# Performance work log

Hardware: AMD Instinct MI355X
Metric: run time of the kernel (lower is better)

Reference implementation:

```python
import jax, jax.numpy as jnp
import numpy as np


def setup_inputs() -> dict:
    key = jax.random.key(0)
    k1, _ = jax.random.split(key)
    N = 4096
    states = jax.random.normal(k1, (N, 8), dtype=jnp.float32)
    log_tau = jnp.log(jnp.asarray(0.05, dtype=jnp.float32))
    return {"states": states, "log_tau": log_tau}


def reference(states, log_tau):
    N = states.shape[0]
    tau = jnp.exp(log_tau)
    pos = (states[:, :2] + states[:, 2:4]) / 2.0   # [N, 2]
    vel = (states[:, 4:6] + states[:, 6:8]) / 2.0  # [N, 2]
    dpos = pos[:, None, :] - pos[None, :, :]       # [N, N, 2]
    dvel = vel[:, None, :] - vel[None, :, :]       # [N, N, 2]
    f_ij = jnp.concatenate([dpos, dvel], axis=-1)  # [N, N, 4]
    dist = jnp.sqrt(jnp.sum(dpos ** 2, axis=-1) + 1e-08)  # [N, N]
    eye = jnp.eye(N, dtype=bool)
    logits = jnp.where(eye, -1e9, -dist / tau)
    alpha = jax.nn.softmax(logits, axis=-1)        # [N, N]
    mu = jnp.einsum('ij,ijd->id', alpha, f_ij)     # [N, 4]
    diff2 = (f_ij - mu[:, None, :]) ** 2           # [N, N, 4]
    sigma = jnp.sqrt(jnp.einsum('ij,ijd->id', alpha, diff2) + 1e-06)  # [N, 4]
    group_vel = jnp.broadcast_to(jnp.mean(vel, axis=0, keepdims=True), (N, 2))
    vel_dev = vel - group_vel
    return jnp.concatenate([mu, sigma, group_vel, vel_dev], axis=-1)  # [N, 12]
```

## Files before the change

kernel.cpp:

```cpp
#include <hip/hip_runtime.h>
#include <math.h>

typedef float v2f __attribute__((ext_vector_type(2)));

#define N_PTS 4096
#define BLOCK 512
#define RPB 4
#define CHUNK 2048
#define SLICES (BLOCK / RPB)
#define JPS (CHUNK / SLICES)
#define PPT (CHUNK / BLOCK)

__global__ __launch_bounds__(BLOCK, 6) void fused_kernel(
        const float* __restrict__ states,
        const float* __restrict__ log_tau_p,
        float* __restrict__ out) {
    __shared__ float4 pvs[CHUNK];
    __shared__ float wsum[8][2];
    __shared__ float red[8][RPB][10];

    const int tid  = threadIdx.x;
    const int lane = tid & 63;
    const int wave = tid >> 6;

    const float s    = __expf(-log_tau_p[0]) * 1.4426950408889634f;
    const float eps2 = 1e-8f * s * s;

    const int rowg = blockIdx.x * RPB + (lane & 3);
    const float4 r0 = *reinterpret_cast<const float4*>(states + rowg * 8);
    const float4 r1 = *reinterpret_cast<const float4*>(states + rowg * 8 + 4);
    const v2f pis = { (r0.x + r0.z) * 0.5f * s, (r0.y + r0.w) * 0.5f * s };
    const v2f piv = { (r1.x + r1.z) * 0.5f,     (r1.y + r1.w) * 0.5f };

    const int slice = wave * (SLICES / 8) + (lane >> 2);

    float l = 0.f, svx = 0.f, svy = 0.f;
    v2f S1p = {0.f, 0.f}, S1v = {0.f, 0.f}, S2p = {0.f, 0.f}, S2v = {0.f, 0.f};

    #pragma unroll
    for (int pass = 0; pass < N_PTS / CHUNK; ++pass) {
        const int J0 = pass * CHUNK;
        #pragma unroll
        for (int k = 0; k < PPT; ++k) {
            const int p = tid + k * BLOCK;
            const float4 s0 = *reinterpret_cast<const float4*>(states + (J0 + p) * 8);
            const float4 s1 = *reinterpret_cast<const float4*>(states + (J0 + p) * 8 + 4);
            float4 e;
            e.x = (s0.x + s0.z) * 0.5f * s;
            e.y = (s0.y + s0.w) * 0.5f * s;
            e.z = (s1.x + s1.z) * 0.5f;
            e.w = (s1.y + s1.w) * 0.5f;
            pvs[p] = e;
            svx += e.z; svy += e.w;
        }
        __syncthreads();

        #pragma unroll 8
        for (int tt = 0; tt < JPS; ++tt) {
            const float4 q = pvs[slice + tt * SLICES];
            v2f dp = { pis.x - q.x, pis.y - q.y };
            v2f dv = { piv.x - q.z, piv.y - q.w };
            float d2 = fmaf(dp.x, dp.x, fmaf(dp.y, dp.y, eps2));
            float w  = __builtin_amdgcn_exp2f(-__builtin_amdgcn_sqrtf(d2));
            l += w;
            v2f wv = { w, w };
            v2f t0 = dp * wv;
            v2f t1 = dv * wv;
            S1p += t0;
            S1v += t1;
            S2p += t0 * dp;
            S2v += t1 * dv;
        }
        __syncthreads();
    }

    float tx = svx, ty = svy;
    #pragma unroll
    for (int off = 32; off; off >>= 1) {
        tx += __shfl_down(tx, off);
        ty += __shfl_down(ty, off);
    }
    if (lane == 0) { wsum[wave][0] = tx; wsum[wave][1] = ty; }

    #pragma unroll
    for (int off = 4; off < 64; off <<= 1) {
        l     += __shfl_xor(l, off);
        S1p.x += __shfl_xor(S1p.x, off);
        S1p.y += __shfl_xor(S1p.y, off);
        S1v.x += __shfl_xor(S1v.x, off);
        S1v.y += __shfl_xor(S1v.y, off);
        S2p.x += __shfl_xor(S2p.x, off);
        S2p.y += __shfl_xor(S2p.y, off);
        S2v.x += __shfl_xor(S2v.x, off);
        S2v.y += __shfl_xor(S2v.y, off);
    }
    if (lane < RPB) {
        float* rr = red[wave][lane];
        rr[0] = l;
        rr[1] = S1p.x; rr[2] = S1p.y; rr[3] = S1v.x; rr[4] = S1v.y;
        rr[5] = S2p.x; rr[6] = S2p.y; rr[7] = S2v.x; rr[8] = S2v.y;
    }
    __syncthreads();

    if (tid < RPB) {
        float acc[9];
        #pragma unroll
        for (int cc = 0; cc < 9; ++cc) acc[cc] = red[0][tid][cc];
        #pragma unroll
        for (int wv = 1; wv < 8; ++wv)
            #pragma unroll
            for (int cc = 0; cc < 9; ++cc) acc[cc] += red[wv][tid][cc];

        const float w_diag = __builtin_amdgcn_exp2f(-__builtin_amdgcn_sqrtf(eps2));
        const float inv_l = 1.0f / (acc[0] - w_diag);
        const float inv_s = 1.0f / s;

        float gvx = 0.f, gvy = 0.f;
        #pragma unroll
        for (int wv = 0; wv < 8; ++wv) { gvx += wsum[wv][0]; gvy += wsum[wv][1]; }
        gvx *= (1.0f / N_PTS);
        gvy *= (1.0f / N_PTS);

        const int row = blockIdx.x * RPB + tid;
        const float4 q1 = *reinterpret_cast<const float4*>(states + row * 8 + 4);
        const float rvx = (q1.x + q1.z) * 0.5f;
        const float rvy = (q1.y + q1.w) * 0.5f;

        float mu[4], sg[4];
        mu[0] = acc[1] * inv_l * inv_s;
        mu[1] = acc[2] * inv_l * inv_s;
        mu[2] = acc[3] * inv_l;
        mu[3] = acc[4] * inv_l;
        const float inv_s2 = inv_s * inv_s;
        float e2[4];
        e2[0] = acc[5] * inv_l * inv_s2;
        e2[1] = acc[6] * inv_l * inv_s2;
        e2[2] = acc[7] * inv_l;
        e2[3] = acc[8] * inv_l;
        #pragma unroll
        for (int d = 0; d < 4; ++d)
            sg[d] = __builtin_amdgcn_sqrtf(fmaf(-mu[d], mu[d], e2[d]) + 1e-6f);

        float4* o = reinterpret_cast<float4*>(out + row * 12);
        o[0] = make_float4(mu[0], mu[1], mu[2], mu[3]);
        o[1] = make_float4(sg[0], sg[1], sg[2], sg[3]);
        o[2] = make_float4(gvx, gvy, rvx - gvx, rvy - gvy);
    }
}

extern "C" void kernel_launch(void* const* d_in, const int* in_sizes, int n_in,
                              void* d_out, int out_size, void* d_ws, size_t ws_size,
                              hipStream_t stream) {
    const float* states  = (const float*)d_in[0];
    const float* log_tau = (const float*)d_in[1];
    float* out = (float*)d_out;
    fused_kernel<<<N_PTS / RPB, BLOCK, 0, stream>>>(states, log_tau, out);
}
```

Before: 70.32 us.

## Register-block all four rows per thread to reuse each shared-memory load

Each thread now holds all four query rows in registers and loops over its own j points, so every float4 read from LDS is reused across four rows instead of one. This cuts LDS traffic by about four times relative to the math. The cost is much more register pressure (36 accumulators plus row data) under the launch bound of 6, and a longer end-of-kernel reduction, since every row now needs a full 64-lane shuffle reduction instead of a partial one.

```diff
diff --git a/kernel.cpp b/kernel.cpp
--- a/kernel.cpp
+++ b/kernel.cpp
@@ -7,9 +7,8 @@
 #define BLOCK 512
 #define RPB 4
 #define CHUNK 2048
-#define SLICES (BLOCK / RPB)
-#define JPS (CHUNK / SLICES)
 #define PPT (CHUNK / BLOCK)
+#define NPASS (N_PTS / CHUNK)
 
 __global__ __launch_bounds__(BLOCK, 6) void fused_kernel(
         const float* __restrict__ states,
@@ -17,7 +16,7 @@
         float* __restrict__ out) {
     __shared__ float4 pvs[CHUNK];
     __shared__ float wsum[8][2];
-    __shared__ float red[8][RPB][10];
+    __shared__ float red[8][RPB][9];
 
     const int tid  = threadIdx.x;
     const int lane = tid & 63;
@@ -26,19 +25,29 @@
     const float s    = __expf(-log_tau_p[0]) * 1.4426950408889634f;
     const float eps2 = 1e-8f * s * s;
 
-    const int rowg = blockIdx.x * RPB + (lane & 3);
-    const float4 r0 = *reinterpret_cast<const float4*>(states + rowg * 8);
-    const float4 r1 = *reinterpret_cast<const float4*>(states + rowg * 8 + 4);
-    const v2f pis = { (r0.x + r0.z) * 0.5f * s, (r0.y + r0.w) * 0.5f * s };
-    const v2f piv = { (r1.x + r1.z) * 0.5f,     (r1.y + r1.w) * 0.5f };
+    v2f pis[RPB], piv[RPB];
+    #pragma unroll
+    for (int r = 0; r < RPB; ++r) {
+        const int rowg = blockIdx.x * RPB + r;
+        const float4 a = *reinterpret_cast<const float4*>(states + rowg * 8);
+        const float4 b = *reinterpret_cast<const float4*>(states + rowg * 8 + 4);
+        pis[r].x = (a.x + a.z) * 0.5f * s;
+        pis[r].y = (a.y + a.w) * 0.5f * s;
+        piv[r].x = (b.x + b.z) * 0.5f;
+        piv[r].y = (b.y + b.w) * 0.5f;
+    }
 
-    const int slice = wave * (SLICES / 8) + (lane >> 2);
+    float l[RPB];
+    v2f S1p[RPB], S1v[RPB], S2p[RPB], S2v[RPB];
+    #pragma unroll
+    for (int r = 0; r < RPB; ++r) {
+        l[r] = 0.f;
+        S1p[r] = (v2f){0.f, 0.f}; S1v[r] = (v2f){0.f, 0.f};
+        S2p[r] = (v2f){0.f, 0.f}; S2v[r] = (v2f){0.f, 0.f};
+    }
+    float svx = 0.f, svy = 0.f;
 
-    float l = 0.f, svx = 0.f, svy = 0.f;
-    v2f S1p = {0.f, 0.f}, S1v = {0.f, 0.f}, S2p = {0.f, 0.f}, S2v = {0.f, 0.f};
-
-    #pragma unroll
-    for (int pass = 0; pass < N_PTS / CHUNK; ++pass) {
+    for (int pass = 0; pass < NPASS; ++pass) {
         const int J0 = pass * CHUNK;
         #pragma unroll
         for (int k = 0; k < PPT; ++k) {
@@ -55,21 +64,24 @@
         }
         __syncthreads();
 
-        #pragma unroll 8
-        for (int tt = 0; tt < JPS; ++tt) {
-            const float4 q = pvs[slice + tt * SLICES];
-            v2f dp = { pis.x - q.x, pis.y - q.y };
-            v2f dv = { piv.x - q.z, piv.y - q.w };
-            float d2 = fmaf(dp.x, dp.x, fmaf(dp.y, dp.y, eps2));
-            float w  = __builtin_amdgcn_exp2f(-__builtin_amdgcn_sqrtf(d2));
-            l += w;
-            v2f wv = { w, w };
-            v2f t0 = dp * wv;
-            v2f t1 = dv * wv;
-            S1p += t0;
-            S1v += t1;
-            S2p += t0 * dp;
-            S2v += t1 * dv;
+        #pragma unroll 2
+        for (int k = 0; k < PPT; ++k) {
+            const float4 q = pvs[tid + k * BLOCK];
+            #pragma unroll
+            for (int r = 0; r < RPB; ++r) {
+                v2f dp = { pis[r].x - q.x, pis[r].y - q.y };
+                v2f dv = { piv[r].x - q.z, piv[r].y - q.w };
+                float d2 = fmaf(dp.x, dp.x, fmaf(dp.y, dp.y, eps2));
+                float w  = __builtin_amdgcn_exp2f(-__builtin_amdgcn_sqrtf(d2));
+                l[r] += w;
+                v2f wv = { w, w };
+                v2f t0 = dp * wv;
+                v2f t1 = dv * wv;
+                S1p[r] += t0;
+                S1v[r] += t1;
+                S2p[r] += t0 * dp;
+                S2v[r] += t1 * dv;
+            }
         }
         __syncthreads();
     }
@@ -83,22 +95,25 @@
     if (lane == 0) { wsum[wave][0] = tx; wsum[wave][1] = ty; }
 
     #pragma unroll
-    for (int off = 4; off < 64; off <<= 1) {
-        l     += __shfl_xor(l, off);
-        S1p.x += __shfl_xor(S1p.x, off);
-        S1p.y += __shfl_xor(S1p.y, off);
-        S1v.x += __shfl_xor(S1v.x, off);
-        S1v.y += __shfl_xor(S1v.y, off);
-        S2p.x += __shfl_xor(S2p.x, off);
-        S2p.y += __shfl_xor(S2p.y, off);
-        S2v.x += __shfl_xor(S2v.x, off);
-        S2v.y += __shfl_xor(S2v.y, off);
-    }
-    if (lane < RPB) {
-        float* rr = red[wave][lane];
-        rr[0] = l;
-        rr[1] = S1p.x; rr[2] = S1p.y; rr[3] = S1v.x; rr[4] = S1v.y;
-        rr[5] = S2p.x; rr[6] = S2p.y; rr[7] = S2v.x; rr[8] = S2v.y;
+    for (int r = 0; r < RPB; ++r) {
+        #pragma unroll
+        for (int off = 32; off; off >>= 1) {
+            l[r]     += __shfl_down(l[r], off);
+            S1p[r].x += __shfl_down(S1p[r].x, off);
+            S1p[r].y += __shfl_down(S1p[r].y, off);
+            S1v[r].x += __shfl_down(S1v[r].x, off);
+            S1v[r].y += __shfl_down(S1v[r].y, off);
+            S2p[r].x += __shfl_down(S2p[r].x, off);
+            S2p[r].y += __shfl_down(S2p[r].y, off);
+            S2v[r].x += __shfl_down(S2v[r].x, off);
+            S2v[r].y += __shfl_down(S2v[r].y, off);
+        }
+        if (lane == 0) {
+            float* rr = red[wave][r];
+            rr[0] = l[r];
+            rr[1] = S1p[r].x; rr[2] = S1p[r].y; rr[3] = S1v[r].x; rr[4] = S1v[r].y;
+            rr[5] = S2p[r].x; rr[6] = S2p[r].y; rr[7] = S2v[r].x; rr[8] = S2v[r].y;
+        }
     }
     __syncthreads();
 
```

Measured after the change: 95.02 us. 35.1% more time.
